# Kernel optimization log

Hardware: AMD Instinct MI355X
Metric: run time of the kernel (lower is better)

Reference implementation:

```python
import jax, jax.numpy as jnp
import numpy as np

B, S, IN, H, NH, PF, L = 8, 1024, 256, 1024, 16, 4096, 6
HD = H // NH
EPS = 1e-5


def _layernorm(x, g, b):
    m = jnp.mean(x, axis=-1, keepdims=True)
    v = jnp.mean((x - m) ** 2, axis=-1, keepdims=True)
    return (x - m) * jax.lax.rsqrt(v + EPS) * g + b


def setup_inputs() -> dict:
    key = jax.random.key(0)
    ks = iter(jax.random.split(key, 40))
    sd = 0.02
    inp = {
        "input_x": jax.random.normal(next(ks), (B, S, IN), jnp.float32),
        "emb_W": jax.random.normal(next(ks), (IN, H), jnp.float32) * sd,
        "emb_b": jnp.zeros((H,), jnp.float32),
        "pos_tab": jax.random.normal(next(ks), (S, H), jnp.float32) * sd,
        "Wq": jax.random.normal(next(ks), (L, H, H), jnp.float32) * sd,
        "bq": jnp.zeros((L, H), jnp.float32),
        "Wk": jax.random.normal(next(ks), (L, H, H), jnp.float32) * sd,
        "bk": jnp.zeros((L, H), jnp.float32),
        "Wv": jax.random.normal(next(ks), (L, H, H), jnp.float32) * sd,
        "bv": jnp.zeros((L, H), jnp.float32),
        "Wo": jax.random.normal(next(ks), (L, H, H), jnp.float32) * sd,
        "bo": jnp.zeros((L, H), jnp.float32),
        "ln1_g": jnp.ones((L, H), jnp.float32),
        "ln1_b": jnp.zeros((L, H), jnp.float32),
        "W1": jax.random.normal(next(ks), (L, H, PF), jnp.float32) * sd,
        "b1": jnp.zeros((L, PF), jnp.float32),
        "W2": jax.random.normal(next(ks), (L, PF, H), jnp.float32) * sd,
        "b2": jnp.zeros((L, H), jnp.float32),
        "ln2_g": jnp.ones((L, H), jnp.float32),
        "ln2_b": jnp.zeros((L, H), jnp.float32),
    }
    return inp


def _encoder(input_x, emb_W, emb_b, pos_tab, Wq, bq, Wk, bk, Wv, bv, Wo, bo,
             ln1_g, ln1_b, W1, b1, W2, b2, ln2_g, ln2_b):
    scale = jnp.sqrt(jnp.float32(H))  # module scales by sqrt(hidden_size)
    x = (input_x @ emb_W + emb_b) * scale + pos_tab[None, :, :]  # [B,S,H]

    def layer(x, p):
        wq, bq_, wk, bk_, wv, bv_, wo, bo_, g1, be1, w1, b1_, w2, b2_, g2, be2 = p
        q = (x @ wq + bq_).reshape(B, S, NH, HD).transpose(0, 2, 1, 3)  # bhsd
        k = (x @ wk + bk_).reshape(B, S, NH, HD).transpose(0, 2, 1, 3)
        v = (x @ wv + bv_).reshape(B, S, NH, HD).transpose(0, 2, 1, 3)
        energy = jnp.einsum("bhqd,bhkd->bhqk", q, k) / scale  # NOTE: /sqrt(H)
        attn = jax.nn.softmax(energy, axis=-1)
        o = jnp.einsum("bhqk,bhkd->bhqd", attn, v)
        o = o.transpose(0, 2, 1, 3).reshape(B, S, H) @ wo + bo_
        x = _layernorm(x + o, g1, be1)
        f = jax.nn.relu(x @ w1 + b1_) @ w2 + b2_
        x = _layernorm(x + f, g2, be2)
        return x, None

    params = (Wq, bq, Wk, bk, Wv, bv, Wo, bo, ln1_g, ln1_b, W1, b1, W2, b2, ln2_g, ln2_b)
    x, _ = jax.lax.scan(layer, x, params)
    return x


def reference(input_x, emb_W, emb_b, pos_tab, Wq, bq, Wk, bk, Wv, bv, Wo, bo,
              ln1_g, ln1_b, W1, b1, W2, b2, ln2_g, ln2_b):
    return _encoder(input_x, emb_W, emb_b, pos_tab, Wq, bq, Wk, bk, Wv, bv,
                    Wo, bo, ln1_g, ln1_b, W1, b1, W2, b2, ln2_g, ln2_b)
```

## Files before the change

### kernel.cpp

```cpp
#include <hip/hip_runtime.h>

#define HDIM 1024
#define BB 8
#define SS 1024
#define NHEAD 16
#define PFF 4096
#define NLAYER 6
#define MM (BB*SS)

typedef __attribute__((ext_vector_type(8))) short bf16x8_t;
typedef __attribute__((ext_vector_type(4))) float f32x4_t;
typedef __attribute__((ext_vector_type(16))) float f32x16_t;

static __device__ __forceinline__ unsigned short f2b(float f) {
  unsigned int u = __float_as_uint(f);
  u += 0x7fffu + ((u >> 16) & 1u);
  return (unsigned short)(u >> 16);
}

static __device__ __forceinline__ unsigned pkbf(float lo, float hi) {
  unsigned r;
  asm("v_cvt_pk_bf16_f32 %0, %1, %2" : "=v"(r) : "v"(lo), "v"(hi));
  return r;
}

static __device__ __forceinline__ bf16x8_t mk8(unsigned a, unsigned b, unsigned c, unsigned d) {
  union { unsigned u[4]; bf16x8_t v; } x;
  x.u[0] = a; x.u[1] = b; x.u[2] = c; x.u[3] = d;
  return x.v;
}

static __device__ __forceinline__ void gload16(const void* g, void* l) {
  __builtin_amdgcn_global_load_lds((__attribute__((address_space(1))) void*)g,
                                   (__attribute__((address_space(3))) void*)l, 16, 0, 0);
}

template<int N>
static __device__ __forceinline__ void vwait() {
  asm volatile("s_waitcnt vmcnt(%0)" :: "n"(N) : "memory");
}

static __device__ __forceinline__ void bar() {
  asm volatile("" ::: "memory");
  __builtin_amdgcn_s_barrier();
  asm volatile("" ::: "memory");
}

__global__ __launch_bounds__(256) void cvt_bf16(const float* __restrict__ in,
                                                unsigned short* __restrict__ o, int n4) {
  const int i = blockIdx.x * 256 + threadIdx.x;
  if (i < n4) {
    const float4 v = ((const float4*)in)[i];
    ushort4 ob = { f2b(v.x), f2b(v.y), f2b(v.z), f2b(v.w) };
    ((ushort4*)o)[i] = ob;
  }
}

__global__ __launch_bounds__(256) void transpose_bf16(const float* __restrict__ in,
                                                      unsigned short* __restrict__ outT,
                                                      int R, int C) {
  __shared__ float tile[32][33];
  const int c0 = blockIdx.x * 32, r0 = blockIdx.y * 32;
  const int tx = threadIdx.x, ty = threadIdx.y;
#pragma unroll
  for (int i = 0; i < 4; ++i)
    tile[ty + 8*i][tx] = in[(size_t)(r0 + ty + 8*i) * C + c0 + tx];
  __syncthreads();
#pragma unroll
  for (int i = 0; i < 4; ++i)
    outT[(size_t)(c0 + ty + 8*i) * R + r0 + tx] = f2b(tile[tx][ty + 8*i]);
}

__global__ __launch_bounds__(256) void vtrans(const unsigned short* __restrict__ qkv,
                                              unsigned short* __restrict__ vt) {
  __shared__ unsigned short tile[32][34];
  const int s0 = blockIdx.x * 32;
  const int by = blockIdx.y;
  const int bh = by >> 1, dt = by & 1;
  const int b = bh >> 4, h = bh & 15;
  const int tx = threadIdx.x, ty = threadIdx.y;
  const unsigned short* src = qkv + ((size_t)(b * 1024 + s0)) * 3072 + 2048 + h * 64 + dt * 32;
#pragma unroll
  for (int i = 0; i < 4; ++i)
    tile[ty + 8*i][tx] = src[(size_t)(ty + 8*i) * 3072 + tx];
  __syncthreads();
  unsigned short* dst = vt + (size_t)(bh * 64 + dt * 32) * 1024 + s0;
#pragma unroll
  for (int i = 0; i < 4; ++i)
    dst[(size_t)(ty + 8*i) * 1024 + tx] = tile[tx][ty + 8*i];
}

__global__ __launch_bounds__(256) void concat_bias(const float* __restrict__ bq,
                                                   const float* __restrict__ bk,
                                                   const float* __restrict__ bv,
                                                   float* __restrict__ o) {
  const int i = blockIdx.x * 256 + threadIdx.x;
  o[i] = (i < 1024) ? bq[i] : ((i < 2048) ? bk[i - 1024] : bv[i - 2048]);
}

template<int BN, bool BIAS, bool RELU, bool RESID, bool EMB, bool WF32, bool WBF16>
__global__ __launch_bounds__(512, 2) void gemm256(
    const unsigned short* __restrict__ A,
    const unsigned short* __restrict__ Bt,
    const float* __restrict__ bias,
    const float* __restrict__ resid,
    const float* __restrict__ pos,
    float* __restrict__ outf,
    unsigned short* __restrict__ outb,
    int M, int N, int K) {
  constexpr int BUFSZ = 32768 + BN * 128;
  constexpr int NJ = BN / 64;
  constexpr int WCN = BN / 4;
  constexpr int BI = BN / 64;
  constexpr int LPT = 4 + BI;
  __shared__ __align__(1024) char smem[2 * BUFSZ];
  const int t = threadIdx.x, lane = t & 63, w = t >> 6;
  const int wr = w >> 2, wc = w & 3;

  int flat = blockIdx.x + gridDim.x * blockIdx.y;
  const int cpx = (gridDim.x * gridDim.y) >> 3;
  flat = (flat & 7) * cpx + (flat >> 3);
  const int m0 = (flat / gridDim.x) * 256;
  const int n0 = (flat % gridDim.x) * BN;

  const f32x4_t z = {0.f, 0.f, 0.f, 0.f};
  f32x4_t acc[8][NJ];
#pragma unroll
  for (int i = 0; i < 8; ++i)
#pragma unroll
    for (int j = 0; j < NJ; ++j) acc[i][j] = z;

  auto stage = [&](int kt, int buf) {
    char* ab_ = smem + buf * BUFSZ;
    char* bb_ = ab_ + 32768;
#pragma unroll
    for (int i = 0; i < 4; ++i) {
      const int chunk = i * 8 + w;
      const int byteoff = chunk * 1024 + lane * 16;
      const int row = byteoff >> 7;
      const int scb = (byteoff & 127) ^ ((row & 7) << 4);
      gload16((const char*)A + ((size_t)(m0 + row) * K + (kt << 6)) * 2 + scb,
              ab_ + chunk * 1024);
    }
#pragma unroll
    for (int i = 0; i < BI; ++i) {
      const int chunk = i * 8 + w;
      const int byteoff = chunk * 1024 + lane * 16;
      const int row = byteoff >> 7;
      const int scb = (byteoff & 127) ^ ((row & 7) << 4);
      gload16((const char*)Bt + ((size_t)(n0 + row) * K + (kt << 6)) * 2 + scb,
              bb_ + chunk * 1024);
    }
  };

  const int nkt = K >> 6;
  stage(0, 0);
  stage(1, 1);
  vwait<LPT>();
  bar();

  int cur = 0;
  for (int kt = 0; kt < nkt; ++kt) {
    const char* ab_ = smem + cur * BUFSZ;
    const char* bb_ = ab_ + 32768;

    bf16x8_t bfr[NJ][2], afr[4][2];
#pragma unroll
    for (int j = 0; j < NJ; ++j)
#pragma unroll
      for (int ks = 0; ks < 2; ++ks) {
        const int row = wc * WCN + j * 16 + (lane & 15);
        const int cb = ks * 64 + ((lane >> 4) << 4);
        bfr[j][ks] = *(const bf16x8_t*)(bb_ + row * 128 + (cb ^ ((row & 7) << 4)));
      }
#pragma unroll
    for (int i = 0; i < 4; ++i)
#pragma unroll
      for (int ks = 0; ks < 2; ++ks) {
        const int row = wr * 128 + i * 16 + (lane & 15);
        const int cb = ks * 64 + ((lane >> 4) << 4);
        afr[i][ks] = *(const bf16x8_t*)(ab_ + row * 128 + (cb ^ ((row & 7) << 4)));
      }
    __builtin_amdgcn_s_setprio(1);
#pragma unroll
    for (int ks = 0; ks < 2; ++ks)
#pragma unroll
      for (int i = 0; i < 4; ++i)
#pragma unroll
        for (int j = 0; j < NJ; ++j)
          acc[i][j] = __builtin_amdgcn_mfma_f32_16x16x32_bf16(afr[i][ks], bfr[j][ks], acc[i][j], 0, 0, 0);
    __builtin_amdgcn_s_setprio(0);
#pragma unroll
    for (int i = 0; i < 4; ++i)
#pragma unroll
      for (int ks = 0; ks < 2; ++ks) {
        const int row = wr * 128 + 64 + i * 16 + (lane & 15);
        const int cb = ks * 64 + ((lane >> 4) << 4);
        afr[i][ks] = *(const bf16x8_t*)(ab_ + row * 128 + (cb ^ ((row & 7) << 4)));
      }
    __builtin_amdgcn_s_setprio(1);
#pragma unroll
    for (int ks = 0; ks < 2; ++ks)
#pragma unroll
      for (int i = 0; i < 4; ++i)
#pragma unroll
        for (int j = 0; j < NJ; ++j)
          acc[4 + i][j] = __builtin_amdgcn_mfma_f32_16x16x32_bf16(afr[i][ks], bfr[j][ks], acc[4 + i][j], 0, 0, 0);
    __builtin_amdgcn_s_setprio(0);

    if (kt + 1 < nkt) {
      bar();
      if (kt + 2 < nkt) {
        stage(kt + 2, cur);
        vwait<LPT>();
      } else {
        vwait<0>();
      }
      bar();
    }
    cur ^= 1;
  }

#pragma unroll
  for (int i = 0; i < 8; ++i) {
    const int rbase = m0 + wr * 128 + i * 16 + ((lane >> 4) << 2);
#pragma unroll
    for (int j = 0; j < NJ; ++j) {
      const int cc = n0 + wc * WCN + j * 16 + (lane & 15);
      float bv = 0.f;
      if (BIAS) bv = bias[cc];
#pragma unroll
      for (int r = 0; r < 4; ++r) {
        const int row = rbase + r;
        float v = acc[i][j][r] + bv;
        if (EMB)  v = v * 32.f + pos[(size_t)(row & (SS - 1)) * N + cc];
        if (RELU) v = fmaxf(v, 0.f);
        if (RESID) v += resid[(size_t)row * N + cc];
        if (WF32)  outf[(size_t)row * N + cc] = v;
        if (WBF16) outb[(size_t)row * N + cc] = f2b(v);
      }
    }
  }
}

__global__ __launch_bounds__(256) void attn2(
    const unsigned short* __restrict__ qkv,
    const unsigned short* __restrict__ vt,
    unsigned short* __restrict__ O) {
  __shared__ __align__(1024) char smem[2 * 16384];
  const int t = threadIdx.x, lane = t & 63, w = t >> 6;
  const int l31 = lane & 31, lg = lane >> 5;
  const int bh = blockIdx.y;
  const int b = bh >> 4, h = bh & 15;
  const size_t rowb = (size_t)b << 10;
  const int q0 = blockIdx.x * 128 + w * 32;

  bf16x8_t qf[4];
  {
    const unsigned short* Qp = qkv + (rowb + q0 + l31) * 3072 + h * 64 + lg * 8;
#pragma unroll
    for (int dd = 0; dd < 4; ++dd) qf[dd] = *(const bf16x8_t*)(Qp + dd * 16);
  }

  f32x16_t oa0, oa1;
#pragma unroll
  for (int r = 0; r < 16; ++r) { oa0[r] = 0.f; oa1[r] = 0.f; }
  float m_run = -1e30f, l_run = 0.f;
  const float inv32 = 1.f / 32.f;

  const char* kglob = (const char*)qkv + ((size_t)1024 + h * 64) * 2;
  const char* vglob = (const char*)vt + (size_t)bh * 64 * 1024 * 2;

  auto stage = [&](int kt, int buf) {
    char* kbuf = smem + buf * 16384;
    char* vbuf = kbuf + 8192;
#pragma unroll
    for (int i = 0; i < 2; ++i) {
      const int chunk = w * 2 + i;
      const int byteoff = chunk * 1024 + lane * 16;
      const int row = byteoff >> 7;
      const int scb = (byteoff & 127) ^ ((row & 7) << 4);
      gload16(kglob + (size_t)(rowb + kt * 64 + row) * 6144 + scb, kbuf + chunk * 1024);
      gload16(vglob + ((size_t)row * 1024 + kt * 64) * 2 + scb,    vbuf + chunk * 1024);
    }
  };

  stage(0, 0);
  for (int kt = 0; kt < 16; ++kt) {
    const int cb = kt & 1;
    __syncthreads();
    if (kt < 15) stage(kt + 1, cb ^ 1);
    const char* kbuf = smem + cb * 16384;
    const char* vbuf = kbuf + 8192;

    f32x16_t p0, p1;
#pragma unroll
    for (int r = 0; r < 16; ++r) { p0[r] = 0.f; p1[r] = 0.f; }
    __builtin_amdgcn_s_setprio(1);
#pragma unroll
    for (int dd = 0; dd < 4; ++dd) {
      {
        const int row = l31;
        const int col = (dd * 32 + (lg << 4)) ^ ((row & 7) << 4);
        bf16x8_t kf = *(const bf16x8_t*)(kbuf + row * 128 + col);
        p0 = __builtin_amdgcn_mfma_f32_32x32x16_bf16(kf, qf[dd], p0, 0, 0, 0);
      }
      {
        const int row = 32 + l31;
        const int col = (dd * 32 + (lg << 4)) ^ ((row & 7) << 4);
        bf16x8_t kf = *(const bf16x8_t*)(kbuf + row * 128 + col);
        p1 = __builtin_amdgcn_mfma_f32_32x32x16_bf16(kf, qf[dd], p1, 0, 0, 0);
      }
    }
    __builtin_amdgcn_s_setprio(0);

    float mx = p0[0];
#pragma unroll
    for (int r = 1; r < 16; ++r) mx = fmaxf(mx, p0[r]);
#pragma unroll
    for (int r = 0; r < 16; ++r) mx = fmaxf(mx, p1[r]);
    mx = fmaxf(mx, __shfl_xor(mx, 32));
    const float mn = fmaxf(m_run, mx * inv32);
    const float fr = __expf(m_run - mn);
    m_run = mn;
    float sum = 0.f;
#pragma unroll
    for (int r = 0; r < 16; ++r) { const float e = __expf(p0[r] * inv32 - mn); p0[r] = e; sum += e; }
#pragma unroll
    for (int r = 0; r < 16; ++r) { const float e = __expf(p1[r] * inv32 - mn); p1[r] = e; sum += e; }
    sum += __shfl_xor(sum, 32);
    l_run = l_run * fr + sum;
#pragma unroll
    for (int r = 0; r < 16; ++r) { oa0[r] *= fr; oa1[r] *= fr; }

    const unsigned A0 = pkbf(p0[0], p0[1]),  B0 = pkbf(p0[2], p0[3]);
    const unsigned C0 = pkbf(p0[4], p0[5]),  D0 = pkbf(p0[6], p0[7]);
    const unsigned E0 = pkbf(p0[8], p0[9]),  F0 = pkbf(p0[10], p0[11]);
    const unsigned G0 = pkbf(p0[12], p0[13]), H0 = pkbf(p0[14], p0[15]);
    const unsigned A1 = pkbf(p1[0], p1[1]),  B1 = pkbf(p1[2], p1[3]);
    const unsigned C1 = pkbf(p1[4], p1[5]),  D1 = pkbf(p1[6], p1[7]);
    const unsigned E1 = pkbf(p1[8], p1[9]),  F1 = pkbf(p1[10], p1[11]);
    const unsigned G1 = pkbf(p1[12], p1[13]), H1 = pkbf(p1[14], p1[15]);
    const unsigned sA0 = __shfl_xor((int)A0, 32), sB0 = __shfl_xor((int)B0, 32);
    const unsigned sC0 = __shfl_xor((int)C0, 32), sD0 = __shfl_xor((int)D0, 32);
    const unsigned sE0 = __shfl_xor((int)E0, 32), sF0 = __shfl_xor((int)F0, 32);
    const unsigned sG0 = __shfl_xor((int)G0, 32), sH0 = __shfl_xor((int)H0, 32);
    const unsigned sA1 = __shfl_xor((int)A1, 32), sB1 = __shfl_xor((int)B1, 32);
    const unsigned sC1 = __shfl_xor((int)C1, 32), sD1 = __shfl_xor((int)D1, 32);
    const unsigned sE1 = __shfl_xor((int)E1, 32), sF1 = __shfl_xor((int)F1, 32);
    const unsigned sG1 = __shfl_xor((int)G1, 32), sH1 = __shfl_xor((int)H1, 32);
    const bool hi = (lg != 0);
    bf16x8_t pf[4];
    pf[0] = hi ? mk8(sC0, sD0, C0, D0) : mk8(A0, B0, sA0, sB0);
    pf[1] = hi ? mk8(sG0, sH0, G0, H0) : mk8(E0, F0, sE0, sF0);
    pf[2] = hi ? mk8(sC1, sD1, C1, D1) : mk8(A1, B1, sA1, sB1);
    pf[3] = hi ? mk8(sG1, sH1, G1, H1) : mk8(E1, F1, sE1, sF1);

    __builtin_amdgcn_s_setprio(1);
#pragma unroll
    for (int c = 0; c < 4; ++c) {
      {
        const int row = l31;
        const int col = (c * 32 + (lg << 4)) ^ ((row & 7) << 4);
        bf16x8_t vf = *(const bf16x8_t*)(vbuf + row * 128 + col);
        oa0 = __builtin_amdgcn_mfma_f32_32x32x16_bf16(vf, pf[c], oa0, 0, 0, 0);
      }
      {
        const int row = 32 + l31;
        const int col = (c * 32 + (lg << 4)) ^ ((row & 7) << 4);
        bf16x8_t vf = *(const bf16x8_t*)(vbuf + row * 128 + col);
        oa1 = __builtin_amdgcn_mfma_f32_32x32x16_bf16(vf, pf[c], oa1, 0, 0, 0);
      }
    }
    __builtin_amdgcn_s_setprio(0);
  }

  const float inv = 1.f / l_run;
  unsigned short* op = O + (rowb + q0 + l31) * 1024 + h * 64 + (lg << 2);
#pragma unroll
  for (int rg = 0; rg < 4; ++rg) {
    const unsigned u0 = pkbf(oa0[rg * 4 + 0] * inv, oa0[rg * 4 + 1] * inv);
    const unsigned u1 = pkbf(oa0[rg * 4 + 2] * inv, oa0[rg * 4 + 3] * inv);
    uint2 st = { u0, u1 };
    *(uint2*)(op + rg * 8) = st;
    const unsigned v0 = pkbf(oa1[rg * 4 + 0] * inv, oa1[rg * 4 + 1] * inv);
    const unsigned v1 = pkbf(oa1[rg * 4 + 2] * inv, oa1[rg * 4 + 3] * inv);
    uint2 st2 = { v0, v1 };
    *(uint2*)(op + 32 + rg * 8) = st2;
  }
}

__global__ __launch_bounds__(256) void ln_kernel(
    const float* __restrict__ y, const float* __restrict__ g, const float* __restrict__ be,
    float* __restrict__ xf, unsigned short* __restrict__ xb) {
  const int row = blockIdx.x;
  const int t = threadIdx.x;
  const float4 v = ((const float4*)(y + (size_t)row * HDIM))[t];
  float s  = v.x + v.y + v.z + v.w;
  float ss = v.x*v.x + v.y*v.y + v.z*v.z + v.w*v.w;
#pragma unroll
  for (int m = 1; m < 64; m <<= 1) { s += __shfl_xor(s, m); ss += __shfl_xor(ss, m); }
  __shared__ float rs[4], rss[4];
  const int w = t >> 6, lane = t & 63;
  if (lane == 0) { rs[w] = s; rss[w] = ss; }
  __syncthreads();
  s  = rs[0] + rs[1] + rs[2] + rs[3];
  ss = rss[0] + rss[1] + rss[2] + rss[3];
  const float mean = s * (1.f / HDIM);
  const float inv = rsqrtf(ss * (1.f / HDIM) - mean * mean + 1e-5f);
  const int c = t * 4;
  const float4 gg = *(const float4*)(g + c);
  const float4 bb = *(const float4*)(be + c);
  float4 o;
  o.x = (v.x - mean) * inv * gg.x + bb.x;
  o.y = (v.y - mean) * inv * gg.y + bb.y;
  o.z = (v.z - mean) * inv * gg.z + bb.z;
  o.w = (v.w - mean) * inv * gg.w + bb.w;
  ((float4*)(xf + (size_t)row * HDIM))[t] = o;
  ushort4 ob = { f2b(o.x), f2b(o.y), f2b(o.z), f2b(o.w) };
  ((ushort4*)(xb + (size_t)row * HDIM))[t] = ob;
}

extern "C" void kernel_launch(void* const* d_in, const int* in_sizes, int n_in,
                              void* d_out, int out_size, void* d_ws, size_t ws_size,
                              hipStream_t stream) {
  const float* input_x = (const float*)d_in[0];
  const float* emb_W   = (const float*)d_in[1];
  const float* emb_b   = (const float*)d_in[2];
  const float* pos_tab = (const float*)d_in[3];
  const float* Wq  = (const float*)d_in[4];
  const float* bq  = (const float*)d_in[5];
  const float* Wk  = (const float*)d_in[6];
  const float* bk  = (const float*)d_in[7];
  const float* Wv  = (const float*)d_in[8];
  const float* bv  = (const float*)d_in[9];
  const float* Wo  = (const float*)d_in[10];
  const float* bo  = (const float*)d_in[11];
  const float* ln1g = (const float*)d_in[12];
  const float* ln1b = (const float*)d_in[13];
  const float* W1  = (const float*)d_in[14];
  const float* b1  = (const float*)d_in[15];
  const float* W2  = (const float*)d_in[16];
  const float* b2  = (const float*)d_in[17];
  const float* ln2g = (const float*)d_in[18];
  const float* ln2b = (const float*)d_in[19];
  float* out = (float*)d_out;

  char* ws = (char*)d_ws;
  size_t off = 0;
  auto alloc = [&](size_t bytes) {
    char* p = ws + off;
    off += (bytes + 255) & ~(size_t)255;
    return p;
  };
  unsigned short* wqkvT = (unsigned short*)alloc((size_t)3072 * HDIM * 2);
  unsigned short* woT   = (unsigned short*)alloc((size_t)HDIM * HDIM * 2);
  unsigned short* w1T   = (unsigned short*)alloc((size_t)PFF * HDIM * 2);
  unsigned short* w2T   = (unsigned short*)alloc((size_t)HDIM * PFF * 2);
  unsigned short* embWT = (unsigned short*)alloc((size_t)HDIM * 256 * 2);
  float*          bqkv  = (float*)alloc(3072 * 4);
  unsigned short* inb   = (unsigned short*)alloc((size_t)MM * 256 * 2);
  unsigned short* xb    = (unsigned short*)alloc((size_t)MM * HDIM * 2);
  unsigned short* qkvb  = (unsigned short*)alloc((size_t)MM * 3072 * 2);
  unsigned short* vtb   = (unsigned short*)alloc((size_t)MM * HDIM * 2);
  unsigned short* ab    = (unsigned short*)alloc((size_t)MM * HDIM * 2);
  float* y = (float*)alloc((size_t)MM * HDIM * 4);
  unsigned short* hb = qkvb;

  const dim3 blk256(256);
  const dim3 blk512(512);
  const dim3 tblk(32, 8);

  cvt_bf16<<<dim3(MM * 256 / 4 / 256), blk256, 0, stream>>>(input_x, inb, MM * 256 / 4);
  transpose_bf16<<<dim3(HDIM / 32, 256 / 32), tblk, 0, stream>>>(emb_W, embWT, 256, HDIM);

  gemm256<128, true, false, false, true, true, true><<<dim3(HDIM / 128, MM / 256), blk512, 0, stream>>>(
      inb, embWT, emb_b, nullptr, pos_tab, out, xb, MM, HDIM, 256);

  for (int l = 0; l < NLAYER; ++l) {
    const size_t wofs = (size_t)l * HDIM * HDIM;
    transpose_bf16<<<dim3(32, 32), tblk, 0, stream>>>(Wq + wofs, wqkvT,               HDIM, HDIM);
    transpose_bf16<<<dim3(32, 32), tblk, 0, stream>>>(Wk + wofs, wqkvT + 1024 * 1024, HDIM, HDIM);
    transpose_bf16<<<dim3(32, 32), tblk, 0, stream>>>(Wv + wofs, wqkvT + 2048 * 1024, HDIM, HDIM);
    transpose_bf16<<<dim3(32, 32), tblk, 0, stream>>>(Wo + wofs, woT, HDIM, HDIM);
    transpose_bf16<<<dim3(PFF / 32, HDIM / 32), tblk, 0, stream>>>(
        W1 + (size_t)l * HDIM * PFF, w1T, HDIM, PFF);
    transpose_bf16<<<dim3(HDIM / 32, PFF / 32), tblk, 0, stream>>>(
        W2 + (size_t)l * PFF * HDIM, w2T, PFF, HDIM);
    concat_bias<<<dim3(12), blk256, 0, stream>>>(bq + l * HDIM, bk + l * HDIM, bv + l * HDIM, bqkv);

    gemm256<256, true, false, false, false, false, true><<<dim3(3072 / 256, MM / 256), blk512, 0, stream>>>(
        xb, wqkvT, bqkv, nullptr, nullptr, nullptr, qkvb, MM, 3072, HDIM);

    vtrans<<<dim3(32, 256), tblk, 0, stream>>>(qkvb, vtb);

    attn2<<<dim3(SS / 128, BB * NHEAD), blk256, 0, stream>>>(qkvb, vtb, ab);

    gemm256<128, true, false, true, false, true, false><<<dim3(HDIM / 128, MM / 256), blk512, 0, stream>>>(
        ab, woT, bo + l * HDIM, out, nullptr, y, nullptr, MM, HDIM, HDIM);
    ln_kernel<<<dim3(MM), blk256, 0, stream>>>(y, ln1g + l * HDIM, ln1b + l * HDIM, out, xb);

    gemm256<256, true, true, false, false, false, true><<<dim3(PFF / 256, MM / 256), blk512, 0, stream>>>(
        xb, w1T, b1 + (size_t)l * PFF, nullptr, nullptr, nullptr, hb, MM, PFF, HDIM);
    gemm256<128, true, false, true, false, true, false><<<dim3(HDIM / 128, MM / 256), blk512, 0, stream>>>(
        hb, w2T, b2 + l * HDIM, out, nullptr, y, nullptr, MM, HDIM, PFF);
    ln_kernel<<<dim3(MM), blk256, 0, stream>>>(y, ln2g + l * HDIM, ln2b + l * HDIM, out, xb);
  }
  (void)in_sizes; (void)n_in; (void)out_size; (void)ws_size;
}
```

Before: 2.280 ms.

## Rewrite GEMM with 32x32 MFMA, 4x2 warp layout and interleaved prefetch

Result: no change. 2.295 ms (+0.7%).

```diff
diff --git a/kernel.cpp b/kernel.cpp
--- a/kernel.cpp
+++ b/kernel.cpp
@@ -99,7 +99,7 @@
 }
 
 template<int BN, bool BIAS, bool RELU, bool RESID, bool EMB, bool WF32, bool WBF16>
-__global__ __launch_bounds__(512, 2) void gemm256(
+__global__ __launch_bounds__(512, 2) void gemm8p(
     const unsigned short* __restrict__ A,
     const unsigned short* __restrict__ Bt,
     const float* __restrict__ bias,
@@ -108,14 +108,12 @@
     float* __restrict__ outf,
     unsigned short* __restrict__ outb,
     int M, int N, int K) {
+  constexpr int NCB = BN / 64;
   constexpr int BUFSZ = 32768 + BN * 128;
-  constexpr int NJ = BN / 64;
-  constexpr int WCN = BN / 4;
-  constexpr int BI = BN / 64;
-  constexpr int LPT = 4 + BI;
   __shared__ __align__(1024) char smem[2 * BUFSZ];
   const int t = threadIdx.x, lane = t & 63, w = t >> 6;
-  const int wr = w >> 2, wc = w & 3;
+  const int l31 = lane & 31, lg = lane >> 5;
+  const int wr = w >> 1, wc = w & 1;
 
   int flat = blockIdx.x + gridDim.x * blockIdx.y;
   const int cpx = (gridDim.x * gridDim.y) >> 3;
@@ -123,116 +121,143 @@
   const int m0 = (flat / gridDim.x) * 256;
   const int n0 = (flat % gridDim.x) * BN;
 
-  const f32x4_t z = {0.f, 0.f, 0.f, 0.f};
-  f32x4_t acc[8][NJ];
-#pragma unroll
-  for (int i = 0; i < 8; ++i)
-#pragma unroll
-    for (int j = 0; j < NJ; ++j) acc[i][j] = z;
-
-  auto stage = [&](int kt, int buf) {
-    char* ab_ = smem + buf * BUFSZ;
-    char* bb_ = ab_ + 32768;
-#pragma unroll
-    for (int i = 0; i < 4; ++i) {
-      const int chunk = i * 8 + w;
-      const int byteoff = chunk * 1024 + lane * 16;
-      const int row = byteoff >> 7;
-      const int scb = (byteoff & 127) ^ ((row & 7) << 4);
-      gload16((const char*)A + ((size_t)(m0 + row) * K + (kt << 6)) * 2 + scb,
-              ab_ + chunk * 1024);
+  const size_t Kb = (size_t)K * 2;
+  const int ric = lane >> 3;
+  const int scb = ((lane & 7) * 16) ^ ((ric & 7) << 4);
+
+  const char* gA0 = (const char*)A  + (size_t)(m0 + wr * 64 + wc * 8 + ric) * Kb + scb;
+  const char* gB0 = (const char*)Bt + (size_t)(n0 + wc * (BN / 2) + wr * 8 + ric) * Kb + scb;
+  const int lA0 = (wr * 64 + wc * 8) * 128;
+  const int lB0 = 32768 + (wc * (BN / 2) + wr * 8) * 128;
+
+  const f32x16_t z16 = {0.f};
+  f32x16_t acc[2][NCB];
+#pragma unroll
+  for (int i = 0; i < 2; ++i)
+#pragma unroll
+    for (int j = 0; j < NCB; ++j) acc[i][j] = z16;
+
+  const int arow = wr * 64 + l31;
+  const int bcol = wc * (BN / 2) + l31;
+  const int sw = (l31 & 7) << 4;
+  const int kx = lg * 16;
+
+  const int nkt = K >> 6;
+
+#define STA(i, kt, buf) gload16(gA0 + (size_t)(i) * 16 * Kb + ((size_t)(kt) << 7), \
+                                smem + (buf) * BUFSZ + lA0 + (i) * 2048)
+#define STB(c, kt, buf) gload16(gB0 + (size_t)(c) * 32 * Kb + ((size_t)(kt) << 7), \
+                                smem + (buf) * BUFSZ + lB0 + (c) * 4096)
+
+  if constexpr (BN == 256) {
+    STB(0, 0, 0); STB(1, 0, 0);
+    STA(0, 0, 0); STA(1, 0, 0);
+    STA(2, 0, 0); STA(3, 0, 0); STB(2, 0, 0); STB(3, 0, 0);
+  } else {
+    STA(0, 0, 0); STA(1, 0, 0); STA(2, 0, 0); STA(3, 0, 0); STB(0, 0, 0);
+    STB(1, 0, 0);
+  }
+
+  bf16x8_t af[2][4];
+  bf16x8_t bfr[2][4];
+
+  for (int kt = 0; kt < nkt; ++kt) {
+    const char* ab = smem + (kt & 1) * BUFSZ;
+    const char* bb = ab + 32768;
+    const int nb = (kt & 1) ^ 1;
+    const bool pf = (kt + 1 < nkt);
+
+    if constexpr (BN == 256) {
+      vwait<4>(); bar();
+      if (pf) { STB(0, kt + 1, nb); STB(1, kt + 1, nb); }
+#pragma unroll
+      for (int ks = 0; ks < 4; ++ks)
+        af[0][ks] = *(const bf16x8_t*)(ab + arow * 128 + ((ks * 32 + kx) ^ sw));
+#pragma unroll
+      for (int c = 0; c < 2; ++c)
+#pragma unroll
+        for (int ks = 0; ks < 4; ++ks)
+          bfr[c][ks] = *(const bf16x8_t*)(bb + (bcol + c * 32) * 128 + ((ks * 32 + kx) ^ sw));
+      __builtin_amdgcn_s_setprio(1);
+#pragma unroll
+      for (int ks = 0; ks < 4; ++ks)
+#pragma unroll
+        for (int c = 0; c < 2; ++c)
+          acc[0][c] = __builtin_amdgcn_mfma_f32_32x32x16_bf16(af[0][ks], bfr[c][ks], acc[0][c], 0, 0, 0);
+      __builtin_amdgcn_s_setprio(0);
+      vwait<2>(); bar();
+      if (pf) { STA(0, kt + 1, nb); STA(1, kt + 1, nb); }
+#pragma unroll
+      for (int ks = 0; ks < 4; ++ks)
+        af[1][ks] = *(const bf16x8_t*)(ab + (arow + 32) * 128 + ((ks * 32 + kx) ^ sw));
+      __builtin_amdgcn_s_setprio(1);
+#pragma unroll
+      for (int ks = 0; ks < 4; ++ks)
+#pragma unroll
+        for (int c = 0; c < 2; ++c)
+          acc[1][c] = __builtin_amdgcn_mfma_f32_32x32x16_bf16(af[1][ks], bfr[c][ks], acc[1][c], 0, 0, 0);
+      __builtin_amdgcn_s_setprio(0);
+      if (pf) { STA(2, kt + 1, nb); STA(3, kt + 1, nb); STB(2, kt + 1, nb); STB(3, kt + 1, nb); }
+#pragma unroll
+      for (int c = 0; c < 2; ++c)
+#pragma unroll
+        for (int ks = 0; ks < 4; ++ks)
+          bfr[c][ks] = *(const bf16x8_t*)(bb + (bcol + (c + 2) * 32) * 128 + ((ks * 32 + kx) ^ sw));
+      __builtin_amdgcn_s_setprio(1);
+#pragma unroll
+      for (int ks = 0; ks < 4; ++ks)
+#pragma unroll
+        for (int c = 0; c < 2; ++c) {
+          acc[0][c + 2] = __builtin_amdgcn_mfma_f32_32x32x16_bf16(af[0][ks], bfr[c][ks], acc[0][c + 2], 0, 0, 0);
+          acc[1][c + 2] = __builtin_amdgcn_mfma_f32_32x32x16_bf16(af[1][ks], bfr[c][ks], acc[1][c + 2], 0, 0, 0);
+        }
+      __builtin_amdgcn_s_setprio(0);
+    } else {
+      vwait<1>(); bar();
+      if (pf) { STA(0, kt + 1, nb); STA(1, kt + 1, nb); STA(2, kt + 1, nb); STA(3, kt + 1, nb); STB(0, kt + 1, nb); }
+#pragma unroll
+      for (int rb = 0; rb < 2; ++rb)
+#pragma unroll
+        for (int ks = 0; ks < 4; ++ks)
+          af[rb][ks] = *(const bf16x8_t*)(ab + (arow + rb * 32) * 128 + ((ks * 32 + kx) ^ sw));
+#pragma unroll
+      for (int ks = 0; ks < 4; ++ks)
+        bfr[0][ks] = *(const bf16x8_t*)(bb + bcol * 128 + ((ks * 32 + kx) ^ sw));
+      __builtin_amdgcn_s_setprio(1);
+#pragma unroll
+      for (int ks = 0; ks < 4; ++ks)
+#pragma unroll
+        for (int rb = 0; rb < 2; ++rb)
+          acc[rb][0] = __builtin_amdgcn_mfma_f32_32x32x16_bf16(af[rb][ks], bfr[0][ks], acc[rb][0], 0, 0, 0);
+      __builtin_amdgcn_s_setprio(0);
+      vwait<5>(); bar();
+      if (pf) { STB(1, kt + 1, nb); }
+#pragma unroll
+      for (int ks = 0; ks < 4; ++ks)
+        bfr[1][ks] = *(const bf16x8_t*)(bb + (bcol + 32) * 128 + ((ks * 32 + kx) ^ sw));
+      __builtin_amdgcn_s_setprio(1);
+#pragma unroll
+      for (int ks = 0; ks < 4; ++ks)
+#pragma unroll
+        for (int rb = 0; rb < 2; ++rb)
+          acc[rb][1] = __builtin_amdgcn_mfma_f32_32x32x16_bf16(af[rb][ks], bfr[1][ks], acc[rb][1], 0, 0, 0);
+      __builtin_amdgcn_s_setprio(0);
     }
-#pragma unroll
-    for (int i = 0; i < BI; ++i) {
-      const int chunk = i * 8 + w;
-      const int byteoff = chunk * 1024 + lane * 16;
-      const int row = byteoff >> 7;
-      const int scb = (byteoff & 127) ^ ((row & 7) << 4);
-      gload16((const char*)Bt + ((size_t)(n0 + row) * K + (kt << 6)) * 2 + scb,
-              bb_ + chunk * 1024);
-    }
-  };
-
-  const int nkt = K >> 6;
-  stage(0, 0);
-  stage(1, 1);
-  vwait<LPT>();
-  bar();
-
-  int cur = 0;
-  for (int kt = 0; kt < nkt; ++kt) {
-    const char* ab_ = smem + cur * BUFSZ;
-    const char* bb_ = ab_ + 32768;
-
-    bf16x8_t bfr[NJ][2], afr[4][2];
-#pragma unroll
-    for (int j = 0; j < NJ; ++j)
-#pragma unroll
-      for (int ks = 0; ks < 2; ++ks) {
-        const int row = wc * WCN + j * 16 + (lane & 15);
-        const int cb = ks * 64 + ((lane >> 4) << 4);
-        bfr[j][ks] = *(const bf16x8_t*)(bb_ + row * 128 + (cb ^ ((row & 7) << 4)));
-      }
-#pragma unroll
-    for (int i = 0; i < 4; ++i)
-#pragma unroll
-      for (int ks = 0; ks < 2; ++ks) {
-        const int row = wr * 128 + i * 16 + (lane & 15);
-        const int cb = ks * 64 + ((lane >> 4) << 4);
-        afr[i][ks] = *(const bf16x8_t*)(ab_ + row * 128 + (cb ^ ((row & 7) << 4)));
-      }
-    __builtin_amdgcn_s_setprio(1);
-#pragma unroll
-    for (int ks = 0; ks < 2; ++ks)
-#pragma unroll
-      for (int i = 0; i < 4; ++i)
-#pragma unroll
-        for (int j = 0; j < NJ; ++j)
-          acc[i][j] = __builtin_amdgcn_mfma_f32_16x16x32_bf16(afr[i][ks], bfr[j][ks], acc[i][j], 0, 0, 0);
-    __builtin_amdgcn_s_setprio(0);
-#pragma unroll
-    for (int i = 0; i < 4; ++i)
-#pragma unroll
-      for (int ks = 0; ks < 2; ++ks) {
-        const int row = wr * 128 + 64 + i * 16 + (lane & 15);
-        const int cb = ks * 64 + ((lane >> 4) << 4);
-        afr[i][ks] = *(const bf16x8_t*)(ab_ + row * 128 + (cb ^ ((row & 7) << 4)));
-      }
-    __builtin_amdgcn_s_setprio(1);
-#pragma unroll
-    for (int ks = 0; ks < 2; ++ks)
-#pragma unroll
-      for (int i = 0; i < 4; ++i)
-#pragma unroll
-        for (int j = 0; j < NJ; ++j)
-          acc[4 + i][j] = __builtin_amdgcn_mfma_f32_16x16x32_bf16(afr[i][ks], bfr[j][ks], acc[4 + i][j], 0, 0, 0);
-    __builtin_amdgcn_s_setprio(0);
-
-    if (kt + 1 < nkt) {
-      bar();
-      if (kt + 2 < nkt) {
-        stage(kt + 2, cur);
-        vwait<LPT>();
-      } else {
-        vwait<0>();
-      }
-      bar();
-    }
-    cur ^= 1;
-  }
-
-#pragma unroll
-  for (int i = 0; i < 8; ++i) {
-    const int rbase = m0 + wr * 128 + i * 16 + ((lane >> 4) << 2);
-#pragma unroll
-    for (int j = 0; j < NJ; ++j) {
-      const int cc = n0 + wc * WCN + j * 16 + (lane & 15);
+  }
+#undef STA
+#undef STB
+
+#pragma unroll
+  for (int rb = 0; rb < 2; ++rb) {
+#pragma unroll
+    for (int cb = 0; cb < NCB; ++cb) {
+      const int cc = n0 + wc * (BN / 2) + cb * 32 + l31;
       float bv = 0.f;
       if (BIAS) bv = bias[cc];
 #pragma unroll
-      for (int r = 0; r < 4; ++r) {
-        const int row = rbase + r;
-        float v = acc[i][j][r] + bv;
+      for (int r = 0; r < 16; ++r) {
+        const int row = m0 + wr * 64 + rb * 32 + (r & 3) + 8 * (r >> 2) + 4 * lg;
+        float v = acc[rb][cb][r] + bv;
         if (EMB)  v = v * 32.f + pos[(size_t)(row & (SS - 1)) * N + cc];
         if (RELU) v = fmaxf(v, 0.f);
         if (RESID) v += resid[(size_t)row * N + cc];
@@ -474,7 +499,7 @@
   cvt_bf16<<<dim3(MM * 256 / 4 / 256), blk256, 0, stream>>>(input_x, inb, MM * 256 / 4);
   transpose_bf16<<<dim3(HDIM / 32, 256 / 32), tblk, 0, stream>>>(emb_W, embWT, 256, HDIM);
 
-  gemm256<128, true, false, false, true, true, true><<<dim3(HDIM / 128, MM / 256), blk512, 0, stream>>>(
+  gemm8p<128, true, false, false, true, true, true><<<dim3(HDIM / 128, MM / 256), blk512, 0, stream>>>(
       inb, embWT, emb_b, nullptr, pos_tab, out, xb, MM, HDIM, 256);
 
   for (int l = 0; l < NLAYER; ++l) {
@@ -489,20 +514,20 @@
         W2 + (size_t)l * PFF * HDIM, w2T, PFF, HDIM);
     concat_bias<<<dim3(12), blk256, 0, stream>>>(bq + l * HDIM, bk + l * HDIM, bv + l * HDIM, bqkv);
 
-    gemm256<256, true, false, false, false, false, true><<<dim3(3072 / 256, MM / 256), blk512, 0, stream>>>(
+    gemm8p<256, true, false, false, false, false, true><<<dim3(3072 / 256, MM / 256), blk512, 0, stream>>>(
         xb, wqkvT, bqkv, nullptr, nullptr, nullptr, qkvb, MM, 3072, HDIM);
 
     vtrans<<<dim3(32, 256), tblk, 0, stream>>>(qkvb, vtb);
 
     attn2<<<dim3(SS / 128, BB * NHEAD), blk256, 0, stream>>>(qkvb, vtb, ab);
 
-    gemm256<128, true, false, true, false, true, false><<<dim3(HDIM / 128, MM / 256), blk512, 0, stream>>>(
+    gemm8p<128, true, false, true, false, true, false><<<dim3(HDIM / 128, MM / 256), blk512, 0, stream>>>(
         ab, woT, bo + l * HDIM, out, nullptr, y, nullptr, MM, HDIM, HDIM);
     ln_kernel<<<dim3(MM), blk256, 0, stream>>>(y, ln1g + l * HDIM, ln1b + l * HDIM, out, xb);
 
-    gemm256<256, true, true, false, false, false, true><<<dim3(PFF / 256, MM / 256), blk512, 0, stream>>>(
+    gemm8p<256, true, true, false, false, false, true><<<dim3(PFF / 256, MM / 256), blk512, 0, stream>>>(
         xb, w1T, b1 + (size_t)l * PFF, nullptr, nullptr, nullptr, hb, MM, PFF, HDIM);
-    gemm256<128, true, false, true, false, true, false><<<dim3(HDIM / 128, MM / 256), blk512, 0, stream>>>(
+    gemm8p<128, true, false, true, false, true, false><<<dim3(HDIM / 128, MM / 256), blk512, 0, stream>>>(
         hb, w2T, b2 + l * HDIM, out, nullptr, y, nullptr, MM, HDIM, PFF);
     ln_kernel<<<dim3(MM), blk256, 0, stream>>>(y, ln2g + l * HDIM, ln2b + l * HDIM, out, xb);
   }
```

## Interleave next-tile global loads with MFMA phases in GEMM main loop

Applied to the files above, without the earlier changes.

After: 2.239 ms. About the same (-1.8%).

```diff
diff --git a/kernel.cpp b/kernel.cpp
--- a/kernel.cpp
+++ b/kernel.cpp
@@ -99,7 +99,7 @@
 }
 
 template<int BN, bool BIAS, bool RELU, bool RESID, bool EMB, bool WF32, bool WBF16>
-__global__ __launch_bounds__(512, 2) void gemm256(
+__global__ __launch_bounds__(512, 2) void gemm4p(
     const unsigned short* __restrict__ A,
     const unsigned short* __restrict__ Bt,
     const float* __restrict__ bias,
@@ -108,11 +108,9 @@
     float* __restrict__ outf,
     unsigned short* __restrict__ outb,
     int M, int N, int K) {
-  constexpr int BUFSZ = 32768 + BN * 128;
   constexpr int NJ = BN / 64;
   constexpr int WCN = BN / 4;
-  constexpr int BI = BN / 64;
-  constexpr int LPT = 4 + BI;
+  constexpr int BUFSZ = 32768 + BN * 128;
   __shared__ __align__(1024) char smem[2 * BUFSZ];
   const int t = threadIdx.x, lane = t & 63, w = t >> 6;
   const int wr = w >> 2, wc = w & 3;
@@ -130,95 +128,150 @@
 #pragma unroll
     for (int j = 0; j < NJ; ++j) acc[i][j] = z;
 
-  auto stage = [&](int kt, int buf) {
-    char* ab_ = smem + buf * BUFSZ;
-    char* bb_ = ab_ + 32768;
-#pragma unroll
-    for (int i = 0; i < 4; ++i) {
-      const int chunk = i * 8 + w;
-      const int byteoff = chunk * 1024 + lane * 16;
-      const int row = byteoff >> 7;
-      const int scb = (byteoff & 127) ^ ((row & 7) << 4);
-      gload16((const char*)A + ((size_t)(m0 + row) * K + (kt << 6)) * 2 + scb,
-              ab_ + chunk * 1024);
+  auto stageA = [&](int i, int kt, int buf) {
+    const int chunk = i * 8 + w;
+    const int byteoff = chunk * 1024 + lane * 16;
+    const int row = byteoff >> 7;
+    const int scb = (byteoff & 127) ^ ((row & 7) << 4);
+    gload16((const char*)A + ((size_t)(m0 + row) * K + (kt << 6)) * 2 + scb,
+            smem + buf * BUFSZ + chunk * 1024);
+  };
+  auto stageB = [&](int i, int kt, int buf) {
+    const int chunk = i * 8 + w;
+    const int byteoff = chunk * 1024 + lane * 16;
+    const int row = byteoff >> 7;
+    const int scb = (byteoff & 127) ^ ((row & 7) << 4);
+    gload16((const char*)Bt + ((size_t)(n0 + row) * K + (kt << 6)) * 2 + scb,
+            smem + buf * BUFSZ + 32768 + chunk * 1024);
+  };
+  auto readA = [&](const char* ab, int fi, int ks) {
+    const int row = wr * 128 + fi * 16 + (lane & 15);
+    const int cb = ks * 64 + ((lane >> 4) << 4);
+    return *(const bf16x8_t*)(ab + row * 128 + (cb ^ ((row & 7) << 4)));
+  };
+  auto readB = [&](const char* bb, int j, int ks) {
+    const int row = wc * WCN + j * 16 + (lane & 15);
+    const int cb = ks * 64 + ((lane >> 4) << 4);
+    return *(const bf16x8_t*)(bb + row * 128 + (cb ^ ((row & 7) << 4)));
+  };
+
+  stageB(0, 0, 0); stageB(1, 0, 0);
+  if constexpr (BN == 256) { stageB(2, 0, 0); stageB(3, 0, 0); }
+  stageA(0, 0, 0); stageA(2, 0, 0); stageA(1, 0, 0); stageA(3, 0, 0);
+  vwait<2>(); bar();
+
+  const int nkt = K >> 6;
+  for (int kt = 0; kt < nkt; ++kt) {
+    const char* ab = smem + (kt & 1) * BUFSZ;
+    const char* bb = ab + 32768;
+    const int nb = (kt & 1) ^ 1;
+    const bool pf = (kt + 1 < nkt);
+    bf16x8_t bfr[NJ][2], af[2][2];
+
+    if constexpr (BN == 256) {
+      if (pf) { stageB(0, kt + 1, nb); stageB(1, kt + 1, nb); }
+#pragma unroll
+      for (int j = 0; j < NJ; ++j)
+#pragma unroll
+        for (int ks = 0; ks < 2; ++ks) bfr[j][ks] = readB(bb, j, ks);
+#pragma unroll
+      for (int d = 0; d < 2; ++d)
+#pragma unroll
+        for (int ks = 0; ks < 2; ++ks) af[d][ks] = readA(ab, d, ks);
+      __builtin_amdgcn_s_setprio(1);
+#pragma unroll
+      for (int ks = 0; ks < 2; ++ks)
+#pragma unroll
+        for (int d = 0; d < 2; ++d)
+#pragma unroll
+          for (int j = 0; j < NJ; ++j)
+            acc[d][j] = __builtin_amdgcn_mfma_f32_16x16x32_bf16(af[d][ks], bfr[j][ks], acc[d][j], 0, 0, 0);
+      __builtin_amdgcn_s_setprio(0);
+      bar();
+      if (pf) { stageB(2, kt + 1, nb); stageB(3, kt + 1, nb); stageA(0, kt + 1, nb); }
+#pragma unroll
+      for (int d = 0; d < 2; ++d)
+#pragma unroll
+        for (int ks = 0; ks < 2; ++ks) af[d][ks] = readA(ab, 2 + d, ks);
+      __builtin_amdgcn_s_setprio(1);
+#pragma unroll
+      for (int ks = 0; ks < 2; ++ks)
+#pragma unroll
+        for (int d = 0; d < 2; ++d)
+#pragma unroll
+          for (int j = 0; j < NJ; ++j)
+            acc[2 + d][j] = __builtin_amdgcn_mfma_f32_16x16x32_bf16(af[d][ks], bfr[j][ks], acc[2 + d][j], 0, 0, 0);
+      __builtin_amdgcn_s_setprio(0);
+      if (pf) vwait<5>(); else vwait<0>();
+      bar();
+      if (pf) stageA(2, kt + 1, nb);
+#pragma unroll
+      for (int d = 0; d < 2; ++d)
+#pragma unroll
+        for (int ks = 0; ks < 2; ++ks) af[d][ks] = readA(ab, 4 + d, ks);
+      __builtin_amdgcn_s_setprio(1);
+#pragma unroll
+      for (int ks = 0; ks < 2; ++ks)
+#pragma unroll
+        for (int d = 0; d < 2; ++d)
+#pragma unroll
+          for (int j = 0; j < NJ; ++j)
+            acc[4 + d][j] = __builtin_amdgcn_mfma_f32_16x16x32_bf16(af[d][ks], bfr[j][ks], acc[4 + d][j], 0, 0, 0);
+      __builtin_amdgcn_s_setprio(0);
+      bar();
+      if (pf) { stageA(1, kt + 1, nb); stageA(3, kt + 1, nb); }
+#pragma unroll
+      for (int d = 0; d < 2; ++d)
+#pragma unroll
+        for (int ks = 0; ks < 2; ++ks) af[d][ks] = readA(ab, 6 + d, ks);
+      __builtin_amdgcn_s_setprio(1);
+#pragma unroll
+      for (int ks = 0; ks < 2; ++ks)
+#pragma unroll
+        for (int d = 0; d < 2; ++d)
+#pragma unroll
+          for (int j = 0; j < NJ; ++j)
+            acc[6 + d][j] = __builtin_amdgcn_mfma_f32_16x16x32_bf16(af[d][ks], bfr[j][ks], acc[6 + d][j], 0, 0, 0);
+      __builtin_amdgcn_s_setprio(0);
+      if (pf) { vwait<2>(); bar(); }
+    } else {
+      bf16x8_t af4[4][2];
+      if (pf) { stageB(0, kt + 1, nb); stageB(1, kt + 1, nb); stageA(0, kt + 1, nb); }
+#pragma unroll
+      for (int j = 0; j < NJ; ++j)
+#pragma unroll
+        for (int ks = 0; ks < 2; ++ks) bfr[j][ks] = readB(bb, j, ks);
+#pragma unroll
+      for (int d = 0; d < 4; ++d)
+#pragma unroll
+        for (int ks = 0; ks < 2; ++ks) af4[d][ks] = readA(ab, d, ks);
+      __builtin_amdgcn_s_setprio(1);
+#pragma unroll
+      for (int ks = 0; ks < 2; ++ks)
+#pragma unroll
+        for (int d = 0; d < 4; ++d)
+#pragma unroll
+          for (int j = 0; j < NJ; ++j)
+            acc[d][j] = __builtin_amdgcn_mfma_f32_16x16x32_bf16(af4[d][ks], bfr[j][ks], acc[d][j], 0, 0, 0);
+      __builtin_amdgcn_s_setprio(0);
+      if (pf) vwait<3>(); else vwait<0>();
+      bar();
+      if (pf) { stageA(2, kt + 1, nb); stageA(1, kt + 1, nb); stageA(3, kt + 1, nb); }
+#pragma unroll
+      for (int d = 0; d < 4; ++d)
+#pragma unroll
+        for (int ks = 0; ks < 2; ++ks) af4[d][ks] = readA(ab, 4 + d, ks);
+      __builtin_amdgcn_s_setprio(1);
+#pragma unroll
+      for (int ks = 0; ks < 2; ++ks)
+#pragma unroll
+        for (int d = 0; d < 4; ++d)
+#pragma unroll
+          for (int j = 0; j < NJ; ++j)
+            acc[4 + d][j] = __builtin_amdgcn_mfma_f32_16x16x32_bf16(af4[d][ks], bfr[j][ks], acc[4 + d][j], 0, 0, 0);
+      __builtin_amdgcn_s_setprio(0);
+      if (pf) { vwait<2>(); bar(); }
     }
-#pragma unroll
-    for (int i = 0; i < BI; ++i) {
-      const int chunk = i * 8 + w;
-      const int byteoff = chunk * 1024 + lane * 16;
-      const int row = byteoff >> 7;
-      const int scb = (byteoff & 127) ^ ((row & 7) << 4);
-      gload16((const char*)Bt + ((size_t)(n0 + row) * K + (kt << 6)) * 2 + scb,
-              bb_ + chunk * 1024);
-    }
-  };
-
-  const int nkt = K >> 6;
-  stage(0, 0);
-  stage(1, 1);
-  vwait<LPT>();
-  bar();
-
-  int cur = 0;
-  for (int kt = 0; kt < nkt; ++kt) {
-    const char* ab_ = smem + cur * BUFSZ;
-    const char* bb_ = ab_ + 32768;
-
-    bf16x8_t bfr[NJ][2], afr[4][2];
-#pragma unroll
-    for (int j = 0; j < NJ; ++j)
-#pragma unroll
-      for (int ks = 0; ks < 2; ++ks) {
-        const int row = wc * WCN + j * 16 + (lane & 15);
-        const int cb = ks * 64 + ((lane >> 4) << 4);
-        bfr[j][ks] = *(const bf16x8_t*)(bb_ + row * 128 + (cb ^ ((row & 7) << 4)));
-      }
-#pragma unroll
-    for (int i = 0; i < 4; ++i)
-#pragma unroll
-      for (int ks = 0; ks < 2; ++ks) {
-        const int row = wr * 128 + i * 16 + (lane & 15);
-        const int cb = ks * 64 + ((lane >> 4) << 4);
-        afr[i][ks] = *(const bf16x8_t*)(ab_ + row * 128 + (cb ^ ((row & 7) << 4)));
-      }
-    __builtin_amdgcn_s_setprio(1);
-#pragma unroll
-    for (int ks = 0; ks < 2; ++ks)
-#pragma unroll
-      for (int i = 0; i < 4; ++i)
-#pragma unroll
-        for (int j = 0; j < NJ; ++j)
-          acc[i][j] = __builtin_amdgcn_mfma_f32_16x16x32_bf16(afr[i][ks], bfr[j][ks], acc[i][j], 0, 0, 0);
-    __builtin_amdgcn_s_setprio(0);
-#pragma unroll
-    for (int i = 0; i < 4; ++i)
-#pragma unroll
-      for (int ks = 0; ks < 2; ++ks) {
-        const int row = wr * 128 + 64 + i * 16 + (lane & 15);
-        const int cb = ks * 64 + ((lane >> 4) << 4);
-        afr[i][ks] = *(const bf16x8_t*)(ab_ + row * 128 + (cb ^ ((row & 7) << 4)));
-      }
-    __builtin_amdgcn_s_setprio(1);
-#pragma unroll
-    for (int ks = 0; ks < 2; ++ks)
-#pragma unroll
-      for (int i = 0; i < 4; ++i)
-#pragma unroll
-        for (int j = 0; j < NJ; ++j)
-          acc[4 + i][j] = __builtin_amdgcn_mfma_f32_16x16x32_bf16(afr[i][ks], bfr[j][ks], acc[4 + i][j], 0, 0, 0);
-    __builtin_amdgcn_s_setprio(0);
-
-    if (kt + 1 < nkt) {
-      bar();
-      if (kt + 2 < nkt) {
-        stage(kt + 2, cur);
-        vwait<LPT>();
-      } else {
-        vwait<0>();
-      }
-      bar();
-    }
-    cur ^= 1;
   }
 
 #pragma unroll
@@ -474,7 +527,7 @@
   cvt_bf16<<<dim3(MM * 256 / 4 / 256), blk256, 0, stream>>>(input_x, inb, MM * 256 / 4);
   transpose_bf16<<<dim3(HDIM / 32, 256 / 32), tblk, 0, stream>>>(emb_W, embWT, 256, HDIM);
 
-  gemm256<128, true, false, false, true, true, true><<<dim3(HDIM / 128, MM / 256), blk512, 0, stream>>>(
+  gemm4p<128, true, false, false, true, true, true><<<dim3(HDIM / 128, MM / 256), blk512, 0, stream>>>(
       inb, embWT, emb_b, nullptr, pos_tab, out, xb, MM, HDIM, 256);
 
   for (int l = 0; l < NLAYER; ++l) {
@@ -489,20 +542,20 @@
         W2 + (size_t)l * PFF * HDIM, w2T, PFF, HDIM);
     concat_bias<<<dim3(12), blk256, 0, stream>>>(bq + l * HDIM, bk + l * HDIM, bv + l * HDIM, bqkv);
 
-    gemm256<256, true, false, false, false, false, true><<<dim3(3072 / 256, MM / 256), blk512, 0, stream>>>(
+    gemm4p<256, true, false, false, false, false, true><<<dim3(3072 / 256, MM / 256), blk512, 0, stream>>>(
         xb, wqkvT, bqkv, nullptr, nullptr, nullptr, qkvb, MM, 3072, HDIM);
 
     vtrans<<<dim3(32, 256), tblk, 0, stream>>>(qkvb, vtb);
 
     attn2<<<dim3(SS / 128, BB * NHEAD), blk256, 0, stream>>>(qkvb, vtb, ab);
 
-    gemm256<128, true, false, true, false, true, false><<<dim3(HDIM / 128, MM / 256), blk512, 0, stream>>>(
+    gemm4p<128, true, false, true, false, true, false><<<dim3(HDIM / 128, MM / 256), blk512, 0, stream>>>(
         ab, woT, bo + l * HDIM, out, nullptr, y, nullptr, MM, HDIM, HDIM);
     ln_kernel<<<dim3(MM), blk256, 0, stream>>>(y, ln1g + l * HDIM, ln1b + l * HDIM, out, xb);
 
-    gemm256<256, true, true, false, false, false, true><<<dim3(PFF / 256, MM / 256), blk512, 0, stream>>>(
+    gemm4p<256, true, true, false, false, false, true><<<dim3(PFF / 256, MM / 256), blk512, 0, stream>>>(
         xb, w1T, b1 + (size_t)l * PFF, nullptr, nullptr, nullptr, hb, MM, PFF, HDIM);
-    gemm256<128, true, false, true, false, true, false><<<dim3(HDIM / 128, MM / 256), blk512, 0, stream>>>(
+    gemm4p<128, true, false, true, false, true, false><<<dim3(HDIM / 128, MM / 256), blk512, 0, stream>>>(
         hb, w2T, b2 + l * HDIM, out, nullptr, y, nullptr, MM, HDIM, PFF);
     ln_kernel<<<dim3(MM), blk256, 0, stream>>>(y, ln2g + l * HDIM, ln2b + l * HDIM, out, xb);
   }
```
